# Optimization experiments

Measured on AMD Instinct MI355X. Metric: run time of the kernel, lower is better.

## Reference

```python
import jax, jax.numpy as jnp
import numpy as np

DIM = 256      # in_channels == hidden_channels
INNER = 256    # heads * dim_head
HEADS = 4
DH = 64        # dim_head = hidden_channels // num_heads
EDGE_DIM = 512 # 2 * in_channels
FF = 1024      # 4 * dim ff expansion
DEPTH = 2
OUT = 1
N = 50000      # two stacked graphs of 25000 nodes
E = 100000
HALF = 25000


def setup_inputs() -> dict:
    key = jax.random.key(0)
    ks = iter(jax.random.split(key, 32))

    def lin(fan_in, fan_out):
        w = jax.random.normal(next(ks), (DEPTH, fan_in, fan_out), jnp.float32) * (1.0 / np.sqrt(fan_in))
        b = jnp.zeros((DEPTH, fan_out), jnp.float32)
        return w, b

    x = jax.random.normal(next(ks), (N, DIM), jnp.float32)
    edge_index = jax.random.randint(next(ks), (2, E), 0, HALF, dtype=jnp.int32)
    Wq, bq = lin(DIM, INNER)
    Wkv, bkv = lin(DIM, 2 * INNER)
    We, be = lin(EDGE_DIM, INNER)
    Wo, bo = lin(INNER, DIM)
    W1, b1 = lin(DIM, FF)
    W2, b2 = lin(FF, DIM)
    g_attn = jax.random.normal(next(ks), (DEPTH, 3 * DIM, 1), jnp.float32) * (1.0 / np.sqrt(3 * DIM))
    g_ff = jax.random.normal(next(ks), (DEPTH, 3 * DIM, 1), jnp.float32) * (1.0 / np.sqrt(3 * DIM))
    ln1_g = jnp.ones((DEPTH, DIM), jnp.float32); ln1_b = jnp.zeros((DEPTH, DIM), jnp.float32)
    ln2_g = jnp.ones((DEPTH, DIM), jnp.float32); ln2_b = jnp.zeros((DEPTH, DIM), jnp.float32)
    Wout = jax.random.normal(next(ks), (DIM, OUT), jnp.float32) * (1.0 / np.sqrt(DIM))
    bout = jnp.zeros((OUT,), jnp.float32)
    return dict(x=x, edge_index=edge_index, ln1_g=ln1_g, ln1_b=ln1_b, Wq=Wq, bq=bq,
                Wkv=Wkv, bkv=bkv, We=We, be=be, Wo=Wo, bo=bo, g_attn=g_attn,
                ln2_g=ln2_g, ln2_b=ln2_b, W1=W1, b1=b1, W2=W2, b2=b2, g_ff=g_ff,
                Wout=Wout, bout=bout)


def _layer_norm(x, g, b):
    mu = jnp.mean(x, axis=-1, keepdims=True)
    var = jnp.mean(jnp.square(x - mu), axis=-1, keepdims=True)
    return (x - mu) * jax.lax.rsqrt(var + 1e-5) * g + b


def _gated_residual(x, res, w):
    # gate = sigmoid(Linear_no_bias(cat(x, res, x - res)))
    gate = jax.nn.sigmoid(jnp.concatenate([x, res, x - res], axis=-1) @ w)  # [n,1]
    return x * gate + res * (1.0 - gate)


def _forward(x, edge_index, ln1_g, ln1_b, Wq, bq, Wkv, bkv, We, be, Wo, bo, g_attn,
             ln2_g, ln2_b, W1, b1, W2, b2, g_ff, Wout, bout):
    src, dst = edge_index[0], edge_index[1]
    # edge_attr = cat(x[src], x[dst]) as built in DeepGraphTransformer_mse.forward
    edge_attr = jnp.concatenate([x[src], x[dst]], axis=-1)  # [E, 2*DIM]
    nodes = x
    n = nodes.shape[0]
    scale = DH ** -0.5
    for l in range(DEPTH):
        xn = _layer_norm(nodes, ln1_g[l], ln1_b[l])
        q = xn @ Wq[l] + bq[l]                                   # [n, INNER]
        k, v = jnp.split(xn @ Wkv[l] + bkv[l], 2, axis=-1)       # [n, INNER] each
        e = edge_attr @ We[l] + be[l]                            # [E, INNER]
        qe = q[dst].reshape(-1, HEADS, DH)                       # [E,H,Dh]
        ke = (k[src] + e).reshape(-1, HEADS, DH)
        ve = (v[src] + e).reshape(-1, HEADS, DH)
        sim = jnp.einsum('ehd,ehd->eh', qe, ke) * scale          # [E,H]
        smax = jax.ops.segment_max(sim, dst, num_segments=n)     # [n,H] (-inf for empty)
        ez = jnp.exp(sim - smax[dst])
        denom = jax.ops.segment_sum(ez, dst, num_segments=n)
        attn = ez / denom[dst]                                   # softmax over incoming edges
        agg = jax.ops.segment_sum(attn[:, :, None] * ve, dst, num_segments=n)
        attn_out = agg.reshape(n, INNER) @ Wo[l] + bo[l]         # [n, DIM]
        nodes = _gated_residual(attn_out, nodes, g_attn[l])
        xn2 = _layer_norm(nodes, ln2_g[l], ln2_b[l])
        h = jax.nn.gelu(xn2 @ W1[l] + b1[l], approximate=False) @ W2[l] + b2[l]
        nodes = _gated_residual(h, nodes, g_ff[l])
    z = nodes @ Wout + bout                                      # [n, OUT]
    return z


def reference(x, edge_index, ln1_g, ln1_b, Wq, bq, Wkv, bkv, We, be, Wo, bo, g_attn,
              ln2_g, ln2_b, W1, b1, W2, b2, g_ff, Wout, bout):
    z = _forward(x, edge_index, ln1_g, ln1_b, Wq, bq, Wkv, bkv, We, be, Wo, bo, g_attn,
                 ln2_g, ln2_b, W1, b1, W2, b2, g_ff, Wout, bout)
    half = z.shape[0] // 2
    z_old, z_new = z[:half], z[half:]
    return (z_new.reshape(-1), z_old, z_new)
```

## Files before the change

kernel.cpp:

```cpp
#include <hip/hip_runtime.h>
#include <cmath>

#define N_NODES 50000
#define N_EDGES 100000
#define HALF_N  25000
#define DIM     256
#define NDEPTH  2
#define MAXDEG  64

#define WT_QKVE 0
#define WT_WO   524288
#define WT_W1   589824
#define WT_W2   851968
#define WT_LAYER 1114112

typedef __bf16 bf16;
typedef bf16 bf16x8 __attribute__((ext_vector_type(8)));
typedef bf16 bf16x4 __attribute__((ext_vector_type(4)));
typedef float f32x4 __attribute__((ext_vector_type(4)));

__device__ __forceinline__ void lds_barrier() {
  asm volatile("s_waitcnt lgkmcnt(0)" ::: "memory");
  __builtin_amdgcn_s_barrier();
  __builtin_amdgcn_sched_barrier(0);
}

__device__ __forceinline__ float wave_sum(float v) {
  v += __shfl_xor(v, 1);
  v += __shfl_xor(v, 2);
  v += __shfl_xor(v, 4);
  v += __shfl_xor(v, 8);
  v += __shfl_xor(v, 16);
  v += __shfl_xor(v, 32);
  return v;
}

__device__ __forceinline__ float fast_gelu(float v) {
  float ax = fabsf(v) * 0.70710678118654752f;
  float t = __builtin_amdgcn_rcpf(fmaf(0.3275911f, ax, 1.0f));
  float p = t * fmaf(t, fmaf(t, fmaf(t, fmaf(t, 1.061405429f, -1.453152027f),
                                     1.421413741f), -0.284496736f), 0.254829592f);
  float e = __expf(-ax * ax);
  float erfv = fmaf(-p, e, 1.0f);
  float ph = copysignf(erfv, v);
  return 0.5f * v * (1.0f + ph);
}

__global__ void ln0_kernel(const float* __restrict__ in, const float* __restrict__ g,
                           const float* __restrict__ b, bf16* __restrict__ A2) {
  int row = blockIdx.x * 4 + (threadIdx.x >> 6);
  if (row >= HALF_N) return;
  int lane = threadIdx.x & 63;
  float4 x = reinterpret_cast<const float4*>(in + (size_t)row * DIM)[lane];
  float mu = wave_sum(x.x + x.y + x.z + x.w) * (1.0f / DIM);
  float d0 = x.x - mu, d1 = x.y - mu, d2 = x.z - mu, d3 = x.w - mu;
  float var = wave_sum(d0*d0 + d1*d1 + d2*d2 + d3*d3) * (1.0f / DIM);
  float r = rsqrtf(var + 1e-5f);
  float4 gv = reinterpret_cast<const float4*>(g)[lane];
  float4 bv = reinterpret_cast<const float4*>(b)[lane];
  bf16x4 o;
  o[0] = (bf16)(d0 * r * gv.x + bv.x);
  o[1] = (bf16)(d1 * r * gv.y + bv.y);
  o[2] = (bf16)(d2 * r * gv.z + bv.z);
  o[3] = (bf16)(d3 * r * gv.w + bv.w);
  *reinterpret_cast<bf16x4*>(A2 + (size_t)row * 512 + lane * 4) = o;
}

template<int KK, int NJ>
__global__ __launch_bounds__(256, 2) void gemm_nloop(
    const bf16* __restrict__ A, const bf16* __restrict__ Wp,
    const float* __restrict__ bias, bf16* __restrict__ C, int M) {
  constexpr int STEPS = KK / 64;
  __shared__ bf16x8 As[KK * 8];
  __shared__ bf16 Cs[64 * 128];
  const int tid = threadIdx.x;
  const int lane = tid & 63, wv = tid >> 6;
  const int wr = wv >> 1, wc = wv & 1;
  const int lm = lane & 15, kb = (lane >> 4) & 3;
  const int row0 = blockIdx.x * 64;
#pragma unroll
  for (int i = 0; i < KK / 32; ++i) {
    int idx = tid + i * 256;
    int row = idx & 63, k8 = idx >> 6;
    int rga = row0 + row; if (rga >= M) rga = M - 1;
    As[idx] = *reinterpret_cast<const bf16x8*>(A + (size_t)rga * KK + k8 * 8);
  }
  lds_barrier();
  const bf16x8* wb = reinterpret_cast<const bf16x8*>(Wp) + kb * 128 + wc * 64 + lm;
  for (int jn = 0; jn < NJ; ++jn) {
    f32x4 acc[2][4] = {};
    for (int st = 0; st < STEPS; ++st) {
#pragma unroll
      for (int ks = 0; ks < 2; ++ks) {
        bf16x8 bfr[4], af[2];
#pragma unroll
        for (int ni = 0; ni < 4; ++ni)
          bfr[ni] = wb[(size_t)jn * (KK * 16) + st * 1024 + ks * 512 + ni * 16];
#pragma unroll
        for (int mi = 0; mi < 2; ++mi)
          af[mi] = As[(st * 8 + ks * 4 + kb) * 64 + wr * 32 + mi * 16 + lm];
#pragma unroll
        for (int mi = 0; mi < 2; ++mi)
#pragma unroll
          for (int ni = 0; ni < 4; ++ni)
            acc[mi][ni] = __builtin_amdgcn_mfma_f32_16x16x32_bf16(af[mi], bfr[ni], acc[mi][ni], 0, 0, 0);
      }
    }
    lds_barrier();
#pragma unroll
    for (int ni = 0; ni < 4; ++ni) {
      int c = wc * 64 + ni * 16 + lm;
      float bval = bias[jn * 128 + c];
#pragma unroll
      for (int mi = 0; mi < 2; ++mi)
#pragma unroll
        for (int e = 0; e < 4; ++e) {
          int r = wr * 32 + mi * 16 + kb * 4 + e;
          Cs[r * 128 + c] = (bf16)(acc[mi][ni][e] + bval);
        }
    }
    lds_barrier();
    bf16x8* C8 = reinterpret_cast<bf16x8*>(C);
    const bf16x8* Cs8 = (const bf16x8*)Cs;
#pragma unroll
    for (int i = 0; i < 4; ++i) {
      int idx = tid + i * 256;
      int row = idx >> 4, c8 = idx & 15;
      int grow = row0 + row;
      if (grow < M) C8[(size_t)grow * (NJ * 16) + jn * 16 + c8] = Cs8[row * 16 + c8];
    }
  }
}

__global__ __launch_bounds__(256, 2) void wo_fused(
    const bf16* __restrict__ A, const bf16* __restrict__ Wp,
    const float* __restrict__ bo, const float* __restrict__ gattn,
    const float* __restrict__ ln2g, const float* __restrict__ ln2b,
    float* __restrict__ nodes, bf16* __restrict__ xn, int M) {
  __shared__ bf16x8 As[2048];
  __shared__ bf16 Cs[64 * 256];
  const int tid = threadIdx.x;
  const int lane = tid & 63, wv = tid >> 6;
  const int wr = wv >> 1, wc = wv & 1;
  const int lm = lane & 15, kb = (lane >> 4) & 3;
  const int row0 = blockIdx.x * 64;
#pragma unroll
  for (int i = 0; i < 8; ++i) {
    int idx = tid + i * 256;
    int row = idx & 63, k8 = idx >> 6;
    int rga = row0 + row; if (rga >= M) rga = M - 1;
    As[idx] = *reinterpret_cast<const bf16x8*>(A + (size_t)rga * 256 + k8 * 8);
  }
  lds_barrier();
  const bf16x8* wb = reinterpret_cast<const bf16x8*>(Wp) + kb * 128 + wc * 64 + lm;
  for (int jn = 0; jn < 2; ++jn) {
    f32x4 acc[2][4] = {};
#pragma unroll
    for (int st = 0; st < 4; ++st) {
#pragma unroll
      for (int ks = 0; ks < 2; ++ks) {
        bf16x8 bfr[4], af[2];
#pragma unroll
        for (int ni = 0; ni < 4; ++ni)
          bfr[ni] = wb[jn * 4096 + st * 1024 + ks * 512 + ni * 16];
#pragma unroll
        for (int mi = 0; mi < 2; ++mi)
          af[mi] = As[(st * 8 + ks * 4 + kb) * 64 + wr * 32 + mi * 16 + lm];
#pragma unroll
        for (int mi = 0; mi < 2; ++mi)
#pragma unroll
          for (int ni = 0; ni < 4; ++ni)
            acc[mi][ni] = __builtin_amdgcn_mfma_f32_16x16x32_bf16(af[mi], bfr[ni], acc[mi][ni], 0, 0, 0);
      }
    }
#pragma unroll
    for (int ni = 0; ni < 4; ++ni) {
      int cfull = jn * 128 + wc * 64 + ni * 16 + lm;
      float bval = bo[cfull];
#pragma unroll
      for (int mi = 0; mi < 2; ++mi)
#pragma unroll
        for (int e = 0; e < 4; ++e) {
          int r = wr * 32 + mi * 16 + kb * 4 + e;
          int ch = (cfull >> 3) ^ (r & 7);
          Cs[r * 256 + ch * 8 + (cfull & 7)] = (bf16)(acc[mi][ni][e] + bval);
        }
    }
  }
  lds_barrier();
  for (int pass = 0; pass < 16; ++pass) {
    int r = pass * 4 + wv;
    int grow = row0 + r;
    if (grow >= M) continue;
    int ch = (lane >> 1) ^ (r & 7);
    bf16x4 c4 = *reinterpret_cast<const bf16x4*>(Cs + r * 256 + ch * 8 + (lane & 1) * 4);
    float x0 = (float)c4[0], x1 = (float)c4[1], x2 = (float)c4[2], x3 = (float)c4[3];
    float4 rv = reinterpret_cast<const float4*>(nodes + (size_t)grow * 256)[lane];
    float4 w0 = reinterpret_cast<const float4*>(gattn)[lane];
    float4 w1 = reinterpret_cast<const float4*>(gattn + 256)[lane];
    float4 w2 = reinterpret_cast<const float4*>(gattn + 512)[lane];
    float dot = x0 * (w0.x + w2.x) + rv.x * (w1.x - w2.x)
              + x1 * (w0.y + w2.y) + rv.y * (w1.y - w2.y)
              + x2 * (w0.z + w2.z) + rv.z * (w1.z - w2.z)
              + x3 * (w0.w + w2.w) + rv.w * (w1.w - w2.w);
    dot = wave_sum(dot);
    float gate = 1.0f / (1.0f + __expf(-dot));
    float n0 = fmaf(x0 - rv.x, gate, rv.x);
    float n1 = fmaf(x1 - rv.y, gate, rv.y);
    float n2 = fmaf(x2 - rv.z, gate, rv.z);
    float n3 = fmaf(x3 - rv.w, gate, rv.w);
    float4 o; o.x = n0; o.y = n1; o.z = n2; o.w = n3;
    reinterpret_cast<float4*>(nodes + (size_t)grow * 256)[lane] = o;
    float mu = wave_sum(n0 + n1 + n2 + n3) * (1.0f / DIM);
    float d0 = n0 - mu, d1 = n1 - mu, d2 = n2 - mu, d3 = n3 - mu;
    float var = wave_sum(d0*d0 + d1*d1 + d2*d2 + d3*d3) * (1.0f / DIM);
    float rs = rsqrtf(var + 1e-5f);
    float4 gv = reinterpret_cast<const float4*>(ln2g)[lane];
    float4 bv = reinterpret_cast<const float4*>(ln2b)[lane];
    bf16x4 ob;
    ob[0] = (bf16)(d0 * rs * gv.x + bv.x);
    ob[1] = (bf16)(d1 * rs * gv.y + bv.y);
    ob[2] = (bf16)(d2 * rs * gv.z + bv.z);
    ob[3] = (bf16)(d3 * rs * gv.w + bv.w);
    *reinterpret_cast<bf16x4*>(xn + (size_t)grow * 256 + lane * 4) = ob;
  }
}

template<int LAST>
__global__ __launch_bounds__(512, 4) void ff_fused(
    const bf16* __restrict__ A, const bf16* __restrict__ W1p,
    const float* __restrict__ b1, const bf16* __restrict__ W2p,
    const float* __restrict__ b2, float* __restrict__ nodes,
    const float* __restrict__ gff, const float* __restrict__ ln1g,
    const float* __restrict__ ln1b, bf16* __restrict__ A2,
    const float* __restrict__ Wout, const float* __restrict__ bout,
    float* __restrict__ out, int M) {
  __shared__ char smem[49152];
  bf16x8* Xs = (bf16x8*)smem;
  bf16*   Cs = (bf16*)smem;
  bf16x8* Hs = (bf16x8*)(smem + 32768);
  const int tid = threadIdx.x;
  const int lane = tid & 63, wv = tid >> 6;
  const int wr = wv >> 2, wc = wv & 3;
  const int lm = lane & 15, kb = (lane >> 4) & 3;
  const int row0 = blockIdx.x * 64;
#pragma unroll
  for (int i = 0; i < 4; ++i) {
    int idx = tid + i * 512;
    int row = idx & 63, k8 = idx >> 6;
    int rga = row0 + row; if (rga >= M) rga = M - 1;
    Xs[idx] = *reinterpret_cast<const bf16x8*>(A + (size_t)rga * 256 + k8 * 8);
  }
  lds_barrier();
  const bf16x8* w1b = (const bf16x8*)W1p + kb * 128 + wc * 32 + lm;
  const bf16x8* w2b = (const bf16x8*)W2p + kb * 256 + wc * 64 + lm;
  f32x4 acc[2][4] = {};
  bf16* hsb = (bf16*)Hs;
  for (int j = 0; j < 8; ++j) {
    bf16x8 pf2[8];
#pragma unroll
    for (int ks = 0; ks < 2; ++ks)
#pragma unroll
      for (int ni = 0; ni < 4; ++ni)
        pf2[ks * 4 + ni] = w2b[j * 4096 + ks * 1024 + ni * 16];
    f32x4 acc1[2][2] = {};
#pragma unroll
    for (int half = 0; half < 2; ++half) {
#pragma unroll
      for (int ks = 0; ks < 4; ++ks) {
        bf16x8 bfr[2], af[2];
#pragma unroll
        for (int ni = 0; ni < 2; ++ni)
          bfr[ni] = w1b[j * 4096 + half * 2048 + ks * 512 + ni * 16];
#pragma unroll
        for (int mi = 0; mi < 2; ++mi)
          af[mi] = Xs[(half * 16 + ks * 4 + kb) * 64 + wr * 32 + mi * 16 + lm];
#pragma unroll
        for (int mi = 0; mi < 2; ++mi)
#pragma unroll
          for (int ni = 0; ni < 2; ++ni)
            acc1[mi][ni] = __builtin_amdgcn_mfma_f32_16x16x32_bf16(af[mi], bfr[ni], acc1[mi][ni], 0, 0, 0);
      }
    }
    lds_barrier();
#pragma unroll
    for (int ni = 0; ni < 2; ++ni) {
      int c = wc * 32 + ni * 16 + lm;
      float bval = b1[j * 128 + c];
#pragma unroll
      for (int mi = 0; mi < 2; ++mi)
#pragma unroll
        for (int e = 0; e < 4; ++e) {
          int r = wr * 32 + mi * 16 + kb * 4 + e;
          float v = fast_gelu(acc1[mi][ni][e] + bval);
          hsb[((c >> 3) * 64 + r) * 8 + (c & 7)] = (bf16)v;
        }
    }
    lds_barrier();
#pragma unroll
    for (int h2 = 0; h2 < 2; ++h2) {
#pragma unroll
      for (int ks = 0; ks < 2; ++ks) {
        bf16x8 bfr[4], af[2];
#pragma unroll
        for (int ni = 0; ni < 4; ++ni)
          bfr[ni] = (h2 == 0) ? pf2[ks * 4 + ni]
                              : w2b[j * 4096 + 2048 + ks * 1024 + ni * 16];
#pragma unroll
        for (int mi = 0; mi < 2; ++mi)
          af[mi] = Hs[(h2 * 8 + ks * 4 + kb) * 64 + wr * 32 + mi * 16 + lm];
#pragma unroll
        for (int mi = 0; mi < 2; ++mi)
#pragma unroll
          for (int ni = 0; ni < 4; ++ni)
            acc[mi][ni] = __builtin_amdgcn_mfma_f32_16x16x32_bf16(af[mi], bfr[ni], acc[mi][ni], 0, 0, 0);
      }
    }
  }
#pragma unroll
  for (int ni = 0; ni < 4; ++ni) {
    int c = wc * 64 + ni * 16 + lm;
    float bval = b2[c];
#pragma unroll
    for (int mi = 0; mi < 2; ++mi)
#pragma unroll
      for (int e = 0; e < 4; ++e) {
        int r = wr * 32 + mi * 16 + kb * 4 + e;
        int ch = (c >> 3) ^ (r & 7);
        Cs[r * 256 + ch * 8 + (c & 7)] = (bf16)(acc[mi][ni][e] + bval);
      }
  }
  lds_barrier();
  for (int pass = 0; pass < 8; ++pass) {
    int r = pass * 8 + wv;
    int grow = row0 + r;
    if (grow >= M) continue;
    int ch = (lane >> 1) ^ (r & 7);
    bf16x4 c4 = *reinterpret_cast<const bf16x4*>(Cs + r * 256 + ch * 8 + (lane & 1) * 4);
    float x0 = (float)c4[0], x1 = (float)c4[1], x2 = (float)c4[2], x3 = (float)c4[3];
    float4 rv = reinterpret_cast<const float4*>(nodes + (size_t)grow * 256)[lane];
    float4 w0 = reinterpret_cast<const float4*>(gff)[lane];
    float4 w1 = reinterpret_cast<const float4*>(gff + 256)[lane];
    float4 w2 = reinterpret_cast<const float4*>(gff + 512)[lane];
    float dot = x0 * (w0.x + w2.x) + rv.x * (w1.x - w2.x)
              + x1 * (w0.y + w2.y) + rv.y * (w1.y - w2.y)
              + x2 * (w0.z + w2.z) + rv.z * (w1.z - w2.z)
              + x3 * (w0.w + w2.w) + rv.w * (w1.w - w2.w);
    dot = wave_sum(dot);
    float gate = 1.0f / (1.0f + __expf(-dot));
    float n0 = fmaf(x0 - rv.x, gate, rv.x);
    float n1 = fmaf(x1 - rv.y, gate, rv.y);
    float n2 = fmaf(x2 - rv.z, gate, rv.z);
    float n3 = fmaf(x3 - rv.w, gate, rv.w);
    if (LAST) {
      float4 wo4 = reinterpret_cast<const float4*>(Wout)[lane];
      float z = n0 * wo4.x + n1 * wo4.y + n2 * wo4.z + n3 * wo4.w;
      z = wave_sum(z);
      if (lane == 0) {
        z += bout[0];
        if (grow < HALF_N) {
          out[HALF_N + grow] = z;
        } else {
          int jj = grow - HALF_N;
          out[jj] = z;
          out[2 * HALF_N + jj] = z;
        }
      }
    } else {
      float4 o; o.x = n0; o.y = n1; o.z = n2; o.w = n3;
      reinterpret_cast<float4*>(nodes + (size_t)grow * 256)[lane] = o;
      if (grow < HALF_N) {
        float mu = wave_sum(n0 + n1 + n2 + n3) * (1.0f / DIM);
        float d0 = n0 - mu, d1 = n1 - mu, d2 = n2 - mu, d3 = n3 - mu;
        float var = wave_sum(d0*d0 + d1*d1 + d2*d2 + d3*d3) * (1.0f / DIM);
        float rs = rsqrtf(var + 1e-5f);
        float4 gv = reinterpret_cast<const float4*>(ln1g)[lane];
        float4 bv = reinterpret_cast<const float4*>(ln1b)[lane];
        bf16x4 ob;
        ob[0] = (bf16)(d0 * rs * gv.x + bv.x);
        ob[1] = (bf16)(d1 * rs * gv.y + bv.y);
        ob[2] = (bf16)(d2 * rs * gv.z + bv.z);
        ob[3] = (bf16)(d3 * rs * gv.w + bv.w);
        *reinterpret_cast<bf16x4*>(A2 + (size_t)grow * 512 + lane * 4) = ob;
      }
    }
  }
}

__global__ void ell_build(const int* __restrict__ ei, int* __restrict__ deg,
                          int* __restrict__ ell) {
  int e = blockIdx.x * 256 + threadIdx.x;
  if (e >= N_EDGES) return;
  int s = ei[e], d = ei[N_EDGES + e];
  int pos = atomicAdd(&deg[d], 1);
  if (pos < MAXDEG) ell[d * MAXDEG + pos] = s;
}

__global__ void attn_gather(const int* __restrict__ deg, const int* __restrict__ ell,
                            const bf16* __restrict__ qkv, bf16* __restrict__ agg) {
  int d = blockIdx.x * 4 + (threadIdx.x >> 6);
  if (d >= HALF_N) return;
  int lane = threadIdx.x & 63;
  int cnt = deg[d]; if (cnt > MAXDEG) cnt = MAXDEG;
  const bf16* qr = qkv + (size_t)d * 1024;
  bf16x4 qb = *reinterpret_cast<const bf16x4*>(qr + lane * 4);
  float q0 = (float)qb[0], q1 = (float)qb[1], q2 = (float)qb[2], q3 = (float)qb[3];
  float m = -INFINITY, den = 0.0f, a0 = 0.0f, a1 = 0.0f, a2 = 0.0f, a3 = 0.0f;
  for (int i = 0; i < cnt; ++i) {
    int s = ell[d * MAXDEG + i];
    bf16x8 kv8 = *reinterpret_cast<const bf16x8*>(qkv + (size_t)s * 1024 + 256 + lane * 8);
    float p = q0 * (float)kv8[0] + q1 * (float)kv8[1] +
              q2 * (float)kv8[2] + q3 * (float)kv8[3];
    p += __shfl_xor(p, 1); p += __shfl_xor(p, 2);
    p += __shfl_xor(p, 4); p += __shfl_xor(p, 8);
    float sim = p * 0.125f;
    float nm = fmaxf(m, sim);
    float sc = __expf(m - nm);
    float w  = __expf(sim - nm);
    den = den * sc + w;
    a0 = a0 * sc + w * (float)kv8[4];
    a1 = a1 * sc + w * (float)kv8[5];
    a2 = a2 * sc + w * (float)kv8[6];
    a3 = a3 * sc + w * (float)kv8[7];
    m = nm;
  }
  bf16x4 o;
  if (cnt > 0) {
    float inv = 1.0f / den;
    bf16x4 eb = *reinterpret_cast<const bf16x4*>(qr + 768 + lane * 4);
    o[0] = (bf16)(a0 * inv + (float)eb[0]);
    o[1] = (bf16)(a1 * inv + (float)eb[1]);
    o[2] = (bf16)(a2 * inv + (float)eb[2]);
    o[3] = (bf16)(a3 * inv + (float)eb[3]);
  } else {
    o[0] = (bf16)0.0f; o[1] = (bf16)0.0f; o[2] = (bf16)0.0f; o[3] = (bf16)0.0f;
  }
  *reinterpret_cast<bf16x4*>(agg + (size_t)d * DIM + lane * 4) = o;
}

template<int DO_LN>
__global__ void gr_ln(const float* __restrict__ fb,
                      float* __restrict__ nodes, const float* __restrict__ w,
                      const float* __restrict__ g, const float* __restrict__ b,
                      bf16* __restrict__ xn, int rows) {
  int r = blockIdx.x * 4 + (threadIdx.x >> 6);
  if (r >= rows) return;
  int lane = threadIdx.x & 63;
  float4 f = reinterpret_cast<const float4*>(fb)[lane];
  float x0 = f.x, x1 = f.y, x2 = f.z, x3 = f.w;
  float4 rv = reinterpret_cast<const float4*>(nodes + (size_t)r * DIM)[lane];
  float4 w0 = reinterpret_cast<const float4*>(w)[lane];
  float4 w1 = reinterpret_cast<const float4*>(w + 256)[lane];
  float4 w2 = reinterpret_cast<const float4*>(w + 512)[lane];
  float p = x0 * (w0.x + w2.x) + rv.x * (w1.x - w2.x)
          + x1 * (w0.y + w2.y) + rv.y * (w1.y - w2.y)
          + x2 * (w0.z + w2.z) + rv.z * (w1.z - w2.z)
          + x3 * (w0.w + w2.w) + rv.w * (w1.w - w2.w);
  p = wave_sum(p);
  float gate = 1.0f / (1.0f + __expf(-p));
  float n0 = x0 * gate + rv.x * (1.0f - gate);
  float n1 = x1 * gate + rv.y * (1.0f - gate);
  float n2 = x2 * gate + rv.z * (1.0f - gate);
  float n3 = x3 * gate + rv.w * (1.0f - gate);
  float4 o; o.x = n0; o.y = n1; o.z = n2; o.w = n3;
  reinterpret_cast<float4*>(nodes + (size_t)r * DIM)[lane] = o;
  if (DO_LN) {
    float mu = wave_sum(n0 + n1 + n2 + n3) * (1.0f / DIM);
    float d0 = n0 - mu, d1 = n1 - mu, d2 = n2 - mu, d3 = n3 - mu;
    float var = wave_sum(d0*d0 + d1*d1 + d2*d2 + d3*d3) * (1.0f / DIM);
    float rs = rsqrtf(var + 1e-5f);
    float4 gv = reinterpret_cast<const float4*>(g)[lane];
    float4 bv = reinterpret_cast<const float4*>(b)[lane];
    bf16x4 ob;
    ob[0] = (bf16)(d0 * rs * gv.x + bv.x);
    ob[1] = (bf16)(d1 * rs * gv.y + bv.y);
    ob[2] = (bf16)(d2 * rs * gv.z + bv.z);
    ob[3] = (bf16)(d3 * rs * gv.w + bv.w);
    *reinterpret_cast<bf16x4*>(xn + (size_t)r * DIM + lane * 4) = ob;
  }
}

__global__ void prep_w(const float* __restrict__ Wq, const float* __restrict__ Wkv,
                       const float* __restrict__ We, const float* __restrict__ Wo,
                       const float* __restrict__ W1, const float* __restrict__ W2,
                       bf16* __restrict__ wt) {
  int idx = blockIdx.x * 256 + threadIdx.x;
  if (idx >= 2 * WT_LAYER) return;
  int l = idx / WT_LAYER, r = idx % WT_LAYER;
  float v;
  if (r < 524288) {
    int jn = r >> 16, t = r & 65535;
    int k8 = t >> 10, u = t & 1023, n = u >> 3, e = u & 7;
    int ncol = jn * 128 + n, k = k8 * 8 + e;
    if (ncol < 256) {
      v = (k < 256) ? Wq[l * 65536 + k * 256 + ncol] : 0.0f;
    } else if (ncol < 768) {
      int u2 = ncol - 256;
      int c = (u2 >> 3) * 4 + (u2 & 3);
      int half = (u2 >> 2) & 1;
      if (k < 256) v = Wkv[l * 131072 + k * 512 + half * 256 + c];
      else         v = We[l * 131072 + (k - 256) * 256 + c];
    } else {
      int c = ncol - 768;
      v = (k < 256) ? 0.0f : We[l * 131072 + k * 256 + c];
    }
  } else if (r < 589824) {
    int rr = r - 524288;
    int jn = rr >> 15, t = rr & 32767;
    int k8 = t >> 10, u = t & 1023, n = u >> 3, e = u & 7;
    v = Wo[l * 65536 + (k8 * 8 + e) * 256 + jn * 128 + n];
  } else if (r < 851968) {
    int rr = r - 589824;
    int j = rr >> 15, t = rr & 32767;
    int k8 = t >> 10, u = t & 1023, n = u >> 3, e = u & 7;
    v = W1[l * 262144 + (k8 * 8 + e) * 1024 + j * 128 + n];
  } else {
    int rr = r - 851968;
    int j = rr >> 15, t = rr & 32767;
    int k8 = t >> 11, u = t & 2047, n = u >> 3, e = u & 7;
    v = W2[l * 262144 + (j * 128 + k8 * 8 + e) * 256 + n];
  }
  wt[idx] = (bf16)v;
}

__global__ void prep_bias(const float* __restrict__ bq, const float* __restrict__ bkv,
                          const float* __restrict__ be, float* __restrict__ biasq) {
  int i = blockIdx.x * 256 + threadIdx.x;
  if (i >= 2048) return;
  int l = i >> 10, n = i & 1023;
  float v;
  if (n < 256) v = bq[l * 256 + n];
  else if (n < 768) {
    int u2 = n - 256;
    int c = (u2 >> 3) * 4 + (u2 & 3);
    int half = (u2 >> 2) & 1;
    v = bkv[l * 512 + half * 256 + c];
  } else v = be[l * 256 + (n - 768)];
  biasq[i] = v;
}

__global__ void prep_x(const float* __restrict__ x, bf16* __restrict__ A2) {
  int i = blockIdx.x * 256 + threadIdx.x;
  if (i >= HALF_N * 64) return;
  int row = i >> 6, c = i & 63;
  float4 v = reinterpret_cast<const float4*>(x)[i];
  bf16x4 o;
  o[0] = (bf16)v.x; o[1] = (bf16)v.y; o[2] = (bf16)v.z; o[3] = (bf16)v.w;
  *reinterpret_cast<bf16x4*>(A2 + (size_t)row * 512 + 256 + c * 4) = o;
}

extern "C" void kernel_launch(void* const* d_in, const int* in_sizes, int n_in,
                              void* d_out, int out_size, void* d_ws, size_t ws_size,
                              hipStream_t stream) {
  const float* x     = (const float*)d_in[0];
  const int*   ei    = (const int*)d_in[1];
  const float* ln1_g = (const float*)d_in[2];
  const float* ln1_b = (const float*)d_in[3];
  const float* Wq    = (const float*)d_in[4];
  const float* bq    = (const float*)d_in[5];
  const float* Wkv   = (const float*)d_in[6];
  const float* bkv   = (const float*)d_in[7];
  const float* We    = (const float*)d_in[8];
  const float* be    = (const float*)d_in[9];
  const float* Wo    = (const float*)d_in[10];
  const float* bo    = (const float*)d_in[11];
  const float* g_attn= (const float*)d_in[12];
  const float* ln2_g = (const float*)d_in[13];
  const float* ln2_b = (const float*)d_in[14];
  const float* W1    = (const float*)d_in[15];
  const float* b1    = (const float*)d_in[16];
  const float* W2    = (const float*)d_in[17];
  const float* b2    = (const float*)d_in[18];
  const float* g_ff  = (const float*)d_in[19];
  const float* Wout  = (const float*)d_in[20];
  const float* bout  = (const float*)d_in[21];
  float* out = (float*)d_out;

  char* base = (char*)d_ws;
  float* nodes   = (float*)base;  base += (size_t)N_NODES * DIM * 4;
  bf16*  A2      = (bf16*)base;   base += (size_t)HALF_N * 512 * 2;
  bf16*  xn_bf   = (bf16*)base;   base += (size_t)N_NODES * DIM * 2;
  bf16*  qkv     = (bf16*)base;   base += (size_t)HALF_N * 1024 * 2;
  bf16*  agg     = (bf16*)base;   base += (size_t)HALF_N * DIM * 2;
  bf16*  wt      = (bf16*)base;   base += (size_t)2 * WT_LAYER * 2;
  float* biasq   = (float*)base;  base += 2048 * 4;
  int*   deg     = (int*)base;    base += HALF_N * 4;
  int*   ell     = (int*)base;    base += (size_t)HALF_N * MAXDEG * 4;

  hipMemcpyAsync(nodes, x, (size_t)N_NODES * DIM * sizeof(float),
                 hipMemcpyDeviceToDevice, stream);
  prep_w<<<(2 * WT_LAYER + 255) / 256, 256, 0, stream>>>(Wq, Wkv, We, Wo, W1, W2, wt);
  prep_bias<<<8, 256, 0, stream>>>(bq, bkv, be, biasq);
  prep_x<<<(HALF_N * 64 + 255) / 256, 256, 0, stream>>>(x, A2);
  hipMemsetAsync(deg, 0, HALF_N * sizeof(int), stream);
  ell_build<<<(N_EDGES + 255) / 256, 256, 0, stream>>>(ei, deg, ell);

  const int GP_H = (HALF_N + 63) / 64;
  const int GP_N = (N_NODES + 63) / 64;

  for (int l = 0; l < NDEPTH; ++l) {
    const bf16* wl = wt + (size_t)l * WT_LAYER;
    if (l == 0)
      ln0_kernel<<<(HALF_N + 3) / 4, 256, 0, stream>>>(x, ln1_g, ln1_b, A2);
    gemm_nloop<512, 8><<<GP_H, 256, 0, stream>>>(A2, wl + WT_QKVE, biasq + l * 1024, qkv, HALF_N);
    attn_gather<<<(HALF_N + 3) / 4, 256, 0, stream>>>(deg, ell, qkv, agg);
    wo_fused<<<GP_H, 256, 0, stream>>>(agg, wl + WT_WO, bo + l * DIM,
                                       g_attn + l * 768, ln2_g + l * DIM, ln2_b + l * DIM,
                                       nodes, xn_bf, HALF_N);
    gr_ln<1><<<(HALF_N + 3) / 4, 256, 0, stream>>>(
        bo + l * DIM, nodes + (size_t)HALF_N * DIM, g_attn + l * 768,
        ln2_g + l * DIM, ln2_b + l * DIM, xn_bf + (size_t)HALF_N * DIM, HALF_N);
    if (l < NDEPTH - 1) {
      ff_fused<0><<<GP_N, 512, 0, stream>>>(
          xn_bf, wl + WT_W1, b1 + l * 1024, wl + WT_W2, b2 + l * DIM,
          nodes, g_ff + l * 768, ln1_g + (l + 1) * DIM, ln1_b + (l + 1) * DIM, A2,
          nullptr, nullptr, nullptr, N_NODES);
    } else {
      ff_fused<1><<<GP_N, 512, 0, stream>>>(
          xn_bf, wl + WT_W1, b1 + l * 1024, wl + WT_W2, b2 + l * DIM,
          nodes, g_ff + l * 768, nullptr, nullptr, nullptr,
          Wout, bout, out, N_NODES);
    }
  }
}
```

Baseline: 508.5 us.

## Fold edge projection through Wo and merge second-half gated residual into wo_fused

Softmax weights over incoming edges sum to one, so the edge-embedding term can be folded algebraically: We·Wo is precomputed, and the Wo GEMM now reads a K=512 input (agg plus the raw edge features from A2). This removes 256 output columns from the QKV GEMM and shrinks the qkv buffer. Nodes with no incoming edges fall back to the bias. The second-half gated-residual kernel is merged into wo_fused through an extra block branch. The change also prefetches the first weight fragments in gemm_nloop, preloads residuals in ff_fused, and unrolls the attention gather by two edges. In exchange, the Wo GEMM does twice the K work, and the folded weights are rounded to bf16.

```diff
diff --git a/kernel.cpp b/kernel.cpp
--- a/kernel.cpp
+++ b/kernel.cpp
@@ -9,10 +9,10 @@
 #define MAXDEG  64
 
 #define WT_QKVE 0
-#define WT_WO   524288
-#define WT_W1   589824
-#define WT_W2   851968
-#define WT_LAYER 1114112
+#define WT_WO   393216
+#define WT_W1   524288
+#define WT_W2   786432
+#define WT_LAYER 1048576
 
 typedef __bf16 bf16;
 typedef bf16 bf16x8 __attribute__((ext_vector_type(8)));
@@ -85,17 +85,26 @@
     int rga = row0 + row; if (rga >= M) rga = M - 1;
     As[idx] = *reinterpret_cast<const bf16x8*>(A + (size_t)rga * KK + k8 * 8);
   }
+  const bf16x8* wb = reinterpret_cast<const bf16x8*>(Wp) + kb * 128 + wc * 64 + lm;
+  bf16x8 pfr[4];
+#pragma unroll
+  for (int ni = 0; ni < 4; ++ni) pfr[ni] = wb[ni * 16];
   lds_barrier();
-  const bf16x8* wb = reinterpret_cast<const bf16x8*>(Wp) + kb * 128 + wc * 64 + lm;
   for (int jn = 0; jn < NJ; ++jn) {
     f32x4 acc[2][4] = {};
+#pragma unroll
     for (int st = 0; st < STEPS; ++st) {
 #pragma unroll
       for (int ks = 0; ks < 2; ++ks) {
         bf16x8 bfr[4], af[2];
-#pragma unroll
-        for (int ni = 0; ni < 4; ++ni)
-          bfr[ni] = wb[(size_t)jn * (KK * 16) + st * 1024 + ks * 512 + ni * 16];
+        if (st == 0 && ks == 0) {
+#pragma unroll
+          for (int ni = 0; ni < 4; ++ni) bfr[ni] = pfr[ni];
+        } else {
+#pragma unroll
+          for (int ni = 0; ni < 4; ++ni)
+            bfr[ni] = wb[(size_t)jn * (KK * 16) + st * 1024 + ks * 512 + ni * 16];
+        }
 #pragma unroll
         for (int mi = 0; mi < 2; ++mi)
           af[mi] = As[(st * 8 + ks * 4 + kb) * 64 + wr * 32 + mi * 16 + lm];
@@ -105,6 +114,11 @@
           for (int ni = 0; ni < 4; ++ni)
             acc[mi][ni] = __builtin_amdgcn_mfma_f32_16x16x32_bf16(af[mi], bfr[ni], acc[mi][ni], 0, 0, 0);
       }
+    }
+    if (jn + 1 < NJ) {
+#pragma unroll
+      for (int ni = 0; ni < 4; ++ni)
+        pfr[ni] = wb[(size_t)(jn + 1) * (KK * 16) + ni * 16];
     }
     lds_barrier();
 #pragma unroll
@@ -133,96 +147,151 @@
 }
 
 __global__ __launch_bounds__(256, 2) void wo_fused(
-    const bf16* __restrict__ A, const bf16* __restrict__ Wp,
-    const float* __restrict__ bo, const float* __restrict__ gattn,
-    const float* __restrict__ ln2g, const float* __restrict__ ln2b,
-    float* __restrict__ nodes, bf16* __restrict__ xn, int M) {
+    const bf16* __restrict__ agg, const bf16* __restrict__ A2,
+    const bf16* __restrict__ Wp, const float* __restrict__ bvec,
+    const float* __restrict__ bo, const int* __restrict__ deg,
+    const float* __restrict__ gattn, const float* __restrict__ ln2g,
+    const float* __restrict__ ln2b, float* __restrict__ nodes,
+    bf16* __restrict__ xn, int rows) {
   __shared__ bf16x8 As[2048];
   __shared__ bf16 Cs[64 * 256];
   const int tid = threadIdx.x;
   const int lane = tid & 63, wv = tid >> 6;
-  const int wr = wv >> 1, wc = wv & 1;
-  const int lm = lane & 15, kb = (lane >> 4) & 3;
   const int row0 = blockIdx.x * 64;
-#pragma unroll
-  for (int i = 0; i < 8; ++i) {
-    int idx = tid + i * 256;
-    int row = idx & 63, k8 = idx >> 6;
-    int rga = row0 + row; if (rga >= M) rga = M - 1;
-    As[idx] = *reinterpret_cast<const bf16x8*>(A + (size_t)rga * 256 + k8 * 8);
-  }
-  lds_barrier();
-  const bf16x8* wb = reinterpret_cast<const bf16x8*>(Wp) + kb * 128 + wc * 64 + lm;
-  for (int jn = 0; jn < 2; ++jn) {
-    f32x4 acc[2][4] = {};
-#pragma unroll
-    for (int st = 0; st < 4; ++st) {
-#pragma unroll
-      for (int ks = 0; ks < 2; ++ks) {
-        bf16x8 bfr[4], af[2];
-#pragma unroll
-        for (int ni = 0; ni < 4; ++ni)
-          bfr[ni] = wb[jn * 4096 + st * 1024 + ks * 512 + ni * 16];
+  if (row0 < HALF_N) {
+    const int wr = wv >> 1, wc = wv & 1;
+    const int lm = lane & 15, kb = (lane >> 4) & 3;
+#pragma unroll
+    for (int i = 0; i < 8; ++i) {
+      int idx = tid + i * 256;
+      int row = idx & 63, k8 = idx >> 6;
+      int rga = row0 + row; if (rga >= HALF_N) rga = HALF_N - 1;
+      As[idx] = *reinterpret_cast<const bf16x8*>(agg + (size_t)rga * 256 + k8 * 8);
+    }
+    bf16x8 afx[2][8];
+#pragma unroll
+    for (int mi = 0; mi < 2; ++mi) {
+      int row = row0 + wr * 32 + mi * 16 + lm;
+      if (row >= HALF_N) row = HALF_N - 1;
+      const bf16* pa = A2 + (size_t)row * 512 + 256 + kb * 8;
+#pragma unroll
+      for (int t = 0; t < 8; ++t)
+        afx[mi][t] = *reinterpret_cast<const bf16x8*>(pa + t * 32);
+    }
+    lds_barrier();
+    const bf16x8* wb = reinterpret_cast<const bf16x8*>(Wp) + kb * 128 + wc * 64 + lm;
+    for (int jn = 0; jn < 2; ++jn) {
+      f32x4 acc[2][4] = {};
+#pragma unroll
+      for (int st = 0; st < 8; ++st) {
+#pragma unroll
+        for (int ks = 0; ks < 2; ++ks) {
+          bf16x8 bfr[4], af[2];
+#pragma unroll
+          for (int ni = 0; ni < 4; ++ni)
+            bfr[ni] = wb[jn * 8192 + (st * 8 + ks * 4) * 128 + ni * 16];
+#pragma unroll
+          for (int mi = 0; mi < 2; ++mi)
+            af[mi] = (st < 4) ? As[(st * 8 + ks * 4 + kb) * 64 + wr * 32 + mi * 16 + lm]
+                              : afx[mi][(st - 4) * 2 + ks];
+#pragma unroll
+          for (int mi = 0; mi < 2; ++mi)
+#pragma unroll
+            for (int ni = 0; ni < 4; ++ni)
+              acc[mi][ni] = __builtin_amdgcn_mfma_f32_16x16x32_bf16(af[mi], bfr[ni], acc[mi][ni], 0, 0, 0);
+        }
+      }
+#pragma unroll
+      for (int ni = 0; ni < 4; ++ni) {
+        int cfull = jn * 128 + wc * 64 + ni * 16 + lm;
+        float bval = bvec[cfull];
 #pragma unroll
         for (int mi = 0; mi < 2; ++mi)
-          af[mi] = As[(st * 8 + ks * 4 + kb) * 64 + wr * 32 + mi * 16 + lm];
-#pragma unroll
-        for (int mi = 0; mi < 2; ++mi)
-#pragma unroll
-          for (int ni = 0; ni < 4; ++ni)
-            acc[mi][ni] = __builtin_amdgcn_mfma_f32_16x16x32_bf16(af[mi], bfr[ni], acc[mi][ni], 0, 0, 0);
-      }
-    }
-#pragma unroll
-    for (int ni = 0; ni < 4; ++ni) {
-      int cfull = jn * 128 + wc * 64 + ni * 16 + lm;
-      float bval = bo[cfull];
-#pragma unroll
-      for (int mi = 0; mi < 2; ++mi)
-#pragma unroll
-        for (int e = 0; e < 4; ++e) {
-          int r = wr * 32 + mi * 16 + kb * 4 + e;
-          int ch = (cfull >> 3) ^ (r & 7);
-          Cs[r * 256 + ch * 8 + (cfull & 7)] = (bf16)(acc[mi][ni][e] + bval);
-        }
-    }
-  }
-  lds_barrier();
-  for (int pass = 0; pass < 16; ++pass) {
-    int r = pass * 4 + wv;
-    int grow = row0 + r;
-    if (grow >= M) continue;
-    int ch = (lane >> 1) ^ (r & 7);
-    bf16x4 c4 = *reinterpret_cast<const bf16x4*>(Cs + r * 256 + ch * 8 + (lane & 1) * 4);
-    float x0 = (float)c4[0], x1 = (float)c4[1], x2 = (float)c4[2], x3 = (float)c4[3];
-    float4 rv = reinterpret_cast<const float4*>(nodes + (size_t)grow * 256)[lane];
-    float4 w0 = reinterpret_cast<const float4*>(gattn)[lane];
-    float4 w1 = reinterpret_cast<const float4*>(gattn + 256)[lane];
-    float4 w2 = reinterpret_cast<const float4*>(gattn + 512)[lane];
-    float dot = x0 * (w0.x + w2.x) + rv.x * (w1.x - w2.x)
-              + x1 * (w0.y + w2.y) + rv.y * (w1.y - w2.y)
-              + x2 * (w0.z + w2.z) + rv.z * (w1.z - w2.z)
-              + x3 * (w0.w + w2.w) + rv.w * (w1.w - w2.w);
-    dot = wave_sum(dot);
-    float gate = 1.0f / (1.0f + __expf(-dot));
-    float n0 = fmaf(x0 - rv.x, gate, rv.x);
-    float n1 = fmaf(x1 - rv.y, gate, rv.y);
-    float n2 = fmaf(x2 - rv.z, gate, rv.z);
-    float n3 = fmaf(x3 - rv.w, gate, rv.w);
-    float4 o; o.x = n0; o.y = n1; o.z = n2; o.w = n3;
-    reinterpret_cast<float4*>(nodes + (size_t)grow * 256)[lane] = o;
-    float mu = wave_sum(n0 + n1 + n2 + n3) * (1.0f / DIM);
-    float d0 = n0 - mu, d1 = n1 - mu, d2 = n2 - mu, d3 = n3 - mu;
-    float var = wave_sum(d0*d0 + d1*d1 + d2*d2 + d3*d3) * (1.0f / DIM);
-    float rs = rsqrtf(var + 1e-5f);
-    float4 gv = reinterpret_cast<const float4*>(ln2g)[lane];
-    float4 bv = reinterpret_cast<const float4*>(ln2b)[lane];
-    bf16x4 ob;
-    ob[0] = (bf16)(d0 * rs * gv.x + bv.x);
-    ob[1] = (bf16)(d1 * rs * gv.y + bv.y);
-    ob[2] = (bf16)(d2 * rs * gv.z + bv.z);
-    ob[3] = (bf16)(d3 * rs * gv.w + bv.w);
-    *reinterpret_cast<bf16x4*>(xn + (size_t)grow * 256 + lane * 4) = ob;
+#pragma unroll
+          for (int e = 0; e < 4; ++e) {
+            int r = wr * 32 + mi * 16 + kb * 4 + e;
+            int ch = (cfull >> 3) ^ (r & 7);
+            Cs[r * 256 + ch * 8 + (cfull & 7)] = (bf16)(acc[mi][ni][e] + bval);
+          }
+      }
+    }
+    lds_barrier();
+    for (int pass = 0; pass < 16; ++pass) {
+      int r = pass * 4 + wv;
+      int grow = row0 + r;
+      float x0, x1, x2, x3;
+      if (grow >= HALF_N || deg[grow] == 0) {
+        float4 bo4 = reinterpret_cast<const float4*>(bo)[lane];
+        x0 = bo4.x; x1 = bo4.y; x2 = bo4.z; x3 = bo4.w;
+      } else {
+        int ch = (lane >> 1) ^ (r & 7);
+        bf16x4 c4 = *reinterpret_cast<const bf16x4*>(Cs + r * 256 + ch * 8 + (lane & 1) * 4);
+        x0 = (float)c4[0]; x1 = (float)c4[1]; x2 = (float)c4[2]; x3 = (float)c4[3];
+      }
+      float4 rv = reinterpret_cast<const float4*>(nodes + (size_t)grow * 256)[lane];
+      float4 w0 = reinterpret_cast<const float4*>(gattn)[lane];
+      float4 w1 = reinterpret_cast<const float4*>(gattn + 256)[lane];
+      float4 w2 = reinterpret_cast<const float4*>(gattn + 512)[lane];
+      float dot = x0 * (w0.x + w2.x) + rv.x * (w1.x - w2.x)
+                + x1 * (w0.y + w2.y) + rv.y * (w1.y - w2.y)
+                + x2 * (w0.z + w2.z) + rv.z * (w1.z - w2.z)
+                + x3 * (w0.w + w2.w) + rv.w * (w1.w - w2.w);
+      dot = wave_sum(dot);
+      float gate = 1.0f / (1.0f + __expf(-dot));
+      float n0 = fmaf(x0 - rv.x, gate, rv.x);
+      float n1 = fmaf(x1 - rv.y, gate, rv.y);
+      float n2 = fmaf(x2 - rv.z, gate, rv.z);
+      float n3 = fmaf(x3 - rv.w, gate, rv.w);
+      float4 o; o.x = n0; o.y = n1; o.z = n2; o.w = n3;
+      reinterpret_cast<float4*>(nodes + (size_t)grow * 256)[lane] = o;
+      float mu = wave_sum(n0 + n1 + n2 + n3) * (1.0f / DIM);
+      float d0 = n0 - mu, d1 = n1 - mu, d2 = n2 - mu, d3 = n3 - mu;
+      float var = wave_sum(d0*d0 + d1*d1 + d2*d2 + d3*d3) * (1.0f / DIM);
+      float rs = rsqrtf(var + 1e-5f);
+      float4 gv = reinterpret_cast<const float4*>(ln2g)[lane];
+      float4 bv = reinterpret_cast<const float4*>(ln2b)[lane];
+      bf16x4 ob;
+      ob[0] = (bf16)(d0 * rs * gv.x + bv.x);
+      ob[1] = (bf16)(d1 * rs * gv.y + bv.y);
+      ob[2] = (bf16)(d2 * rs * gv.z + bv.z);
+      ob[3] = (bf16)(d3 * rs * gv.w + bv.w);
+      *reinterpret_cast<bf16x4*>(xn + (size_t)grow * 256 + lane * 4) = ob;
+    }
+  } else {
+    float4 bo4 = reinterpret_cast<const float4*>(bo)[lane];
+    for (int pass = 0; pass < 16; ++pass) {
+      int grow = row0 + pass * 4 + wv;
+      if (grow >= rows) continue;
+      float x0 = bo4.x, x1 = bo4.y, x2 = bo4.z, x3 = bo4.w;
+      float4 rv = reinterpret_cast<const float4*>(nodes + (size_t)grow * 256)[lane];
+      float4 w0 = reinterpret_cast<const float4*>(gattn)[lane];
+      float4 w1 = reinterpret_cast<const float4*>(gattn + 256)[lane];
+      float4 w2 = reinterpret_cast<const float4*>(gattn + 512)[lane];
+      float dot = x0 * (w0.x + w2.x) + rv.x * (w1.x - w2.x)
+                + x1 * (w0.y + w2.y) + rv.y * (w1.y - w2.y)
+                + x2 * (w0.z + w2.z) + rv.z * (w1.z - w2.z)
+                + x3 * (w0.w + w2.w) + rv.w * (w1.w - w2.w);
+      dot = wave_sum(dot);
+      float gate = 1.0f / (1.0f + __expf(-dot));
+      float n0 = fmaf(x0 - rv.x, gate, rv.x);
+      float n1 = fmaf(x1 - rv.y, gate, rv.y);
+      float n2 = fmaf(x2 - rv.z, gate, rv.z);
+      float n3 = fmaf(x3 - rv.w, gate, rv.w);
+      float4 o; o.x = n0; o.y = n1; o.z = n2; o.w = n3;
+      reinterpret_cast<float4*>(nodes + (size_t)grow * 256)[lane] = o;
+      float mu = wave_sum(n0 + n1 + n2 + n3) * (1.0f / DIM);
+      float d0 = n0 - mu, d1 = n1 - mu, d2 = n2 - mu, d3 = n3 - mu;
+      float var = wave_sum(d0*d0 + d1*d1 + d2*d2 + d3*d3) * (1.0f / DIM);
+      float rs = rsqrtf(var + 1e-5f);
+      float4 gv = reinterpret_cast<const float4*>(ln2g)[lane];
+      float4 bv = reinterpret_cast<const float4*>(ln2b)[lane];
+      bf16x4 ob;
+      ob[0] = (bf16)(d0 * rs * gv.x + bv.x);
+      ob[1] = (bf16)(d1 * rs * gv.y + bv.y);
+      ob[2] = (bf16)(d2 * rs * gv.z + bv.z);
+      ob[3] = (bf16)(d3 * rs * gv.w + bv.w);
+      *reinterpret_cast<bf16x4*>(xn + (size_t)grow * 256 + lane * 4) = ob;
+    }
   }
 }
 
@@ -251,6 +320,13 @@
     int rga = row0 + row; if (rga >= M) rga = M - 1;
     Xs[idx] = *reinterpret_cast<const bf16x8*>(A + (size_t)rga * 256 + k8 * 8);
   }
+  float4 rvf[8];
+#pragma unroll
+  for (int pass = 0; pass < 8; ++pass) {
+    int grow = row0 + pass * 8 + wv;
+    if (grow >= M) grow = M - 1;
+    rvf[pass] = reinterpret_cast<const float4*>(nodes + (size_t)grow * 256)[lane];
+  }
   lds_barrier();
   const bf16x8* w1b = (const bf16x8*)W1p + kb * 128 + wc * 32 + lm;
   const bf16x8* w2b = (const bf16x8*)W2p + kb * 256 + wc * 64 + lm;
@@ -338,7 +414,7 @@
     int ch = (lane >> 1) ^ (r & 7);
     bf16x4 c4 = *reinterpret_cast<const bf16x4*>(Cs + r * 256 + ch * 8 + (lane & 1) * 4);
     float x0 = (float)c4[0], x1 = (float)c4[1], x2 = (float)c4[2], x3 = (float)c4[3];
-    float4 rv = reinterpret_cast<const float4*>(nodes + (size_t)grow * 256)[lane];
+    float4 rv = rvf[pass];
     float4 w0 = reinterpret_cast<const float4*>(gff)[lane];
     float4 w1 = reinterpret_cast<const float4*>(gff + 256)[lane];
     float4 w2 = reinterpret_cast<const float4*>(gff + 512)[lane];
@@ -402,21 +478,43 @@
   if (d >= HALF_N) return;
   int lane = threadIdx.x & 63;
   int cnt = deg[d]; if (cnt > MAXDEG) cnt = MAXDEG;
-  const bf16* qr = qkv + (size_t)d * 1024;
+  const bf16* qr = qkv + (size_t)d * 768;
   bf16x4 qb = *reinterpret_cast<const bf16x4*>(qr + lane * 4);
   float q0 = (float)qb[0], q1 = (float)qb[1], q2 = (float)qb[2], q3 = (float)qb[3];
   float m = -INFINITY, den = 0.0f, a0 = 0.0f, a1 = 0.0f, a2 = 0.0f, a3 = 0.0f;
-  for (int i = 0; i < cnt; ++i) {
+  int i = 0;
+  for (; i + 2 <= cnt; i += 2) {
+    int s0 = ell[d * MAXDEG + i];
+    int s1 = ell[d * MAXDEG + i + 1];
+    bf16x8 k0 = *reinterpret_cast<const bf16x8*>(qkv + (size_t)s0 * 768 + 256 + lane * 8);
+    bf16x8 k1 = *reinterpret_cast<const bf16x8*>(qkv + (size_t)s1 * 768 + 256 + lane * 8);
+    float p0 = q0 * (float)k0[0] + q1 * (float)k0[1] + q2 * (float)k0[2] + q3 * (float)k0[3];
+    float p1 = q0 * (float)k1[0] + q1 * (float)k1[1] + q2 * (float)k1[2] + q3 * (float)k1[3];
+    p0 += __shfl_xor(p0, 1); p1 += __shfl_xor(p1, 1);
+    p0 += __shfl_xor(p0, 2); p1 += __shfl_xor(p1, 2);
+    p0 += __shfl_xor(p0, 4); p1 += __shfl_xor(p1, 4);
+    p0 += __shfl_xor(p0, 8); p1 += __shfl_xor(p1, 8);
+    float s0v = p0 * 0.125f, s1v = p1 * 0.125f;
+    float nm = fmaxf(m, fmaxf(s0v, s1v));
+    float sc = __expf(m - nm);
+    float w0 = __expf(s0v - nm), w1 = __expf(s1v - nm);
+    den = den * sc + w0 + w1;
+    a0 = a0 * sc + w0 * (float)k0[4] + w1 * (float)k1[4];
+    a1 = a1 * sc + w0 * (float)k0[5] + w1 * (float)k1[5];
+    a2 = a2 * sc + w0 * (float)k0[6] + w1 * (float)k1[6];
+    a3 = a3 * sc + w0 * (float)k0[7] + w1 * (float)k1[7];
+    m = nm;
+  }
+  if (i < cnt) {
     int s = ell[d * MAXDEG + i];
-    bf16x8 kv8 = *reinterpret_cast<const bf16x8*>(qkv + (size_t)s * 1024 + 256 + lane * 8);
-    float p = q0 * (float)kv8[0] + q1 * (float)kv8[1] +
-              q2 * (float)kv8[2] + q3 * (float)kv8[3];
+    bf16x8 kv8 = *reinterpret_cast<const bf16x8*>(qkv + (size_t)s * 768 + 256 + lane * 8);
+    float p = q0 * (float)kv8[0] + q1 * (float)kv8[1] + q2 * (float)kv8[2] + q3 * (float)kv8[3];
     p += __shfl_xor(p, 1); p += __shfl_xor(p, 2);
     p += __shfl_xor(p, 4); p += __shfl_xor(p, 8);
     float sim = p * 0.125f;
     float nm = fmaxf(m, sim);
     float sc = __expf(m - nm);
-    float w  = __expf(sim - nm);
+    float w = __expf(sim - nm);
     den = den * sc + w;
     a0 = a0 * sc + w * (float)kv8[4];
     a1 = a1 * sc + w * (float)kv8[5];
@@ -427,57 +525,14 @@
   bf16x4 o;
   if (cnt > 0) {
     float inv = 1.0f / den;
-    bf16x4 eb = *reinterpret_cast<const bf16x4*>(qr + 768 + lane * 4);
-    o[0] = (bf16)(a0 * inv + (float)eb[0]);
-    o[1] = (bf16)(a1 * inv + (float)eb[1]);
-    o[2] = (bf16)(a2 * inv + (float)eb[2]);
-    o[3] = (bf16)(a3 * inv + (float)eb[3]);
+    o[0] = (bf16)(a0 * inv);
+    o[1] = (bf16)(a1 * inv);
+    o[2] = (bf16)(a2 * inv);
+    o[3] = (bf16)(a3 * inv);
   } else {
     o[0] = (bf16)0.0f; o[1] = (bf16)0.0f; o[2] = (bf16)0.0f; o[3] = (bf16)0.0f;
   }
   *reinterpret_cast<bf16x4*>(agg + (size_t)d * DIM + lane * 4) = o;
-}
-
-template<int DO_LN>
-__global__ void gr_ln(const float* __restrict__ fb,
-                      float* __restrict__ nodes, const float* __restrict__ w,
-                      const float* __restrict__ g, const float* __restrict__ b,
-                      bf16* __restrict__ xn, int rows) {
-  int r = blockIdx.x * 4 + (threadIdx.x >> 6);
-  if (r >= rows) return;
-  int lane = threadIdx.x & 63;
-  float4 f = reinterpret_cast<const float4*>(fb)[lane];
-  float x0 = f.x, x1 = f.y, x2 = f.z, x3 = f.w;
-  float4 rv = reinterpret_cast<const float4*>(nodes + (size_t)r * DIM)[lane];
-  float4 w0 = reinterpret_cast<const float4*>(w)[lane];
-  float4 w1 = reinterpret_cast<const float4*>(w + 256)[lane];
-  float4 w2 = reinterpret_cast<const float4*>(w + 512)[lane];
-  float p = x0 * (w0.x + w2.x) + rv.x * (w1.x - w2.x)
-          + x1 * (w0.y + w2.y) + rv.y * (w1.y - w2.y)
-          + x2 * (w0.z + w2.z) + rv.z * (w1.z - w2.z)
-          + x3 * (w0.w + w2.w) + rv.w * (w1.w - w2.w);
-  p = wave_sum(p);
-  float gate = 1.0f / (1.0f + __expf(-p));
-  float n0 = x0 * gate + rv.x * (1.0f - gate);
-  float n1 = x1 * gate + rv.y * (1.0f - gate);
-  float n2 = x2 * gate + rv.z * (1.0f - gate);
-  float n3 = x3 * gate + rv.w * (1.0f - gate);
-  float4 o; o.x = n0; o.y = n1; o.z = n2; o.w = n3;
-  reinterpret_cast<float4*>(nodes + (size_t)r * DIM)[lane] = o;
-  if (DO_LN) {
-    float mu = wave_sum(n0 + n1 + n2 + n3) * (1.0f / DIM);
-    float d0 = n0 - mu, d1 = n1 - mu, d2 = n2 - mu, d3 = n3 - mu;
-    float var = wave_sum(d0*d0 + d1*d1 + d2*d2 + d3*d3) * (1.0f / DIM);
-    float rs = rsqrtf(var + 1e-5f);
-    float4 gv = reinterpret_cast<const float4*>(g)[lane];
-    float4 bv = reinterpret_cast<const float4*>(b)[lane];
-    bf16x4 ob;
-    ob[0] = (bf16)(d0 * rs * gv.x + bv.x);
-    ob[1] = (bf16)(d1 * rs * gv.y + bv.y);
-    ob[2] = (bf16)(d2 * rs * gv.z + bv.z);
-    ob[3] = (bf16)(d3 * rs * gv.w + bv.w);
-    *reinterpret_cast<bf16x4*>(xn + (size_t)r * DIM + lane * 4) = ob;
-  }
 }
 
 __global__ void prep_w(const float* __restrict__ Wq, const float* __restrict__ Wkv,
@@ -488,34 +543,33 @@
   if (idx >= 2 * WT_LAYER) return;
   int l = idx / WT_LAYER, r = idx % WT_LAYER;
   float v;
-  if (r < 524288) {
+  if (r < 393216) {
     int jn = r >> 16, t = r & 65535;
     int k8 = t >> 10, u = t & 1023, n = u >> 3, e = u & 7;
     int ncol = jn * 128 + n, k = k8 * 8 + e;
     if (ncol < 256) {
       v = (k < 256) ? Wq[l * 65536 + k * 256 + ncol] : 0.0f;
-    } else if (ncol < 768) {
+    } else {
       int u2 = ncol - 256;
       int c = (u2 >> 3) * 4 + (u2 & 3);
       int half = (u2 >> 2) & 1;
       if (k < 256) v = Wkv[l * 131072 + k * 512 + half * 256 + c];
       else         v = We[l * 131072 + (k - 256) * 256 + c];
-    } else {
-      int c = ncol - 768;
-      v = (k < 256) ? 0.0f : We[l * 131072 + k * 256 + c];
-    }
-  } else if (r < 589824) {
+    }
+  } else if (r < 524288) {
+    int rr = r - 393216;
+    int jn = rr >> 16, t = rr & 65535;
+    int k8 = t >> 10, u = t & 1023, n = u >> 3, e = u & 7;
+    int k = k8 * 8 + e;
+    if (k >= 256) return;
+    v = Wo[l * 65536 + k * 256 + jn * 128 + n];
+  } else if (r < 786432) {
     int rr = r - 524288;
-    int jn = rr >> 15, t = rr & 32767;
-    int k8 = t >> 10, u = t & 1023, n = u >> 3, e = u & 7;
-    v = Wo[l * 65536 + (k8 * 8 + e) * 256 + jn * 128 + n];
-  } else if (r < 851968) {
-    int rr = r - 589824;
     int j = rr >> 15, t = rr & 32767;
     int k8 = t >> 10, u = t & 1023, n = u >> 3, e = u & 7;
     v = W1[l * 262144 + (k8 * 8 + e) * 1024 + j * 128 + n];
   } else {
-    int rr = r - 851968;
+    int rr = r - 786432;
     int j = rr >> 15, t = rr & 32767;
     int k8 = t >> 11, u = t & 2047, n = u >> 3, e = u & 7;
     v = W2[l * 262144 + (j * 128 + k8 * 8 + e) * 256 + n];
@@ -523,19 +577,49 @@
   wt[idx] = (bf16)v;
 }
 
+__global__ void prep_weff(const float* __restrict__ We, const float* __restrict__ Wo,
+                          bf16* __restrict__ wt) {
+  int idx = blockIdx.x * 256 + threadIdx.x;
+  if (idx >= 2 * 65536) return;
+  int l = idx >> 16, r = idx & 65535;
+  int k = r >> 8, n = r & 255;
+  const float* wer = We + l * 131072 + (256 + k) * 256;
+  const float* wor = Wo + l * 65536 + n;
+  float acc = 0.0f;
+#pragma unroll 4
+  for (int m = 0; m < 256; ++m) acc += wer[m] * wor[m * 256];
+  int kf = 256 + k;
+  size_t off = (size_t)l * WT_LAYER + WT_WO +
+               (n >> 7) * 65536 + (kf >> 3) * 1024 + (n & 127) * 8 + (kf & 7);
+  wt[off] = (bf16)acc;
+}
+
+__global__ void prep_bvec(const float* __restrict__ be, const float* __restrict__ Wo,
+                          const float* __restrict__ bo, float* __restrict__ biasq) {
+  int idx = blockIdx.x * 256 + threadIdx.x;
+  if (idx >= 512) return;
+  int l = idx >> 8, n = idx & 255;
+  const float* ber = be + l * 256;
+  const float* wor = Wo + l * 65536 + n;
+  float acc = bo[l * 256 + n];
+#pragma unroll 4
+  for (int m = 0; m < 256; ++m) acc += ber[m] * wor[m * 256];
+  biasq[1536 + l * 256 + n] = acc;
+}
+
 __global__ void prep_bias(const float* __restrict__ bq, const float* __restrict__ bkv,
-                          const float* __restrict__ be, float* __restrict__ biasq) {
+                          float* __restrict__ biasq) {
   int i = blockIdx.x * 256 + threadIdx.x;
-  if (i >= 2048) return;
-  int l = i >> 10, n = i & 1023;
+  if (i >= 1536) return;
+  int l = i / 768, n = i % 768;
   float v;
   if (n < 256) v = bq[l * 256 + n];
-  else if (n < 768) {
+  else {
     int u2 = n - 256;
     int c = (u2 >> 3) * 4 + (u2 & 3);
     int half = (u2 >> 2) & 1;
     v = bkv[l * 512 + half * 256 + c];
-  } else v = be[l * 256 + (n - 768)];
+  }
   biasq[i] = v;
 }
 
@@ -580,7 +664,7 @@
   float* nodes   = (float*)base;  base += (size_t)N_NODES * DIM * 4;
   bf16*  A2      = (bf16*)base;   base += (size_t)HALF_N * 512 * 2;
   bf16*  xn_bf   = (bf16*)base;   base += (size_t)N_NODES * DIM * 2;
-  bf16*  qkv     = (bf16*)base;   base += (size_t)HALF_N * 1024 * 2;
+  bf16*  qkv     = (bf16*)base;   base += (size_t)HALF_N * 768 * 2;
   bf16*  agg     = (bf16*)base;   base += (size_t)HALF_N * DIM * 2;
   bf16*  wt      = (bf16*)base;   base += (size_t)2 * WT_LAYER * 2;
   float* biasq   = (float*)base;  base += 2048 * 4;
@@ -590,7 +674,9 @@
   hipMemcpyAsync(nodes, x, (size_t)N_NODES * DIM * sizeof(float),
                  hipMemcpyDeviceToDevice, stream);
   prep_w<<<(2 * WT_LAYER + 255) / 256, 256, 0, stream>>>(Wq, Wkv, We, Wo, W1, W2, wt);
-  prep_bias<<<8, 256, 0, stream>>>(bq, bkv, be, biasq);
+  prep_weff<<<(2 * 65536 + 255) / 256, 256, 0, stream>>>(We, Wo, wt);
+  prep_bvec<<<2, 256, 0, stream>>>(be, Wo, bo, biasq);
+  prep_bias<<<6, 256, 0, stream>>>(bq, bkv, biasq);
   prep_x<<<(HALF_N * 64 + 255) / 256, 256, 0, stream>>>(x, A2);
   hipMemsetAsync(deg, 0, HALF_N * sizeof(int), stream);
   ell_build<<<(N_EDGES + 255) / 256, 256, 0, stream>>>(ei, deg, ell);
@@ -602,14 +688,12 @@
     const bf16* wl = wt + (size_t)l * WT_LAYER;
     if (l == 0)
       ln0_kernel<<<(HALF_N + 3) / 4, 256, 0, stream>>>(x, ln1_g, ln1_b, A2);
-    gemm_nloop<512, 8><<<GP_H, 256, 0, stream>>>(A2, wl + WT_QKVE, biasq + l * 1024, qkv, HALF_N);
+    gemm_nloop<512, 6><<<GP_H, 256, 0, stream>>>(A2, wl + WT_QKVE, biasq + l * 768, qkv, HALF_N);
     attn_gather<<<(HALF_N + 3) / 4, 256, 0, stream>>>(deg, ell, qkv, agg);
-    wo_fused<<<GP_H, 256, 0, stream>>>(agg, wl + WT_WO, bo + l * DIM,
-                                       g_attn + l * 768, ln2_g + l * DIM, ln2_b + l * DIM,
-                                       nodes, xn_bf, HALF_N);
-    gr_ln<1><<<(HALF_N + 3) / 4, 256, 0, stream>>>(
-        bo + l * DIM, nodes + (size_t)HALF_N * DIM, g_attn + l * 768,
-        ln2_g + l * DIM, ln2_b + l * DIM, xn_bf + (size_t)HALF_N * DIM, HALF_N);
+    wo_fused<<<GP_N, 256, 0, stream>>>(agg, A2, wl + WT_WO, biasq + 1536 + l * 256,
+                                       bo + l * DIM, deg, g_attn + l * 768,
+                                       ln2_g + l * DIM, ln2_b + l * DIM,
+                                       nodes, xn_bf, N_NODES);
     if (l < NDEPTH - 1) {
       ff_fused<0><<<GP_N, 512, 0, stream>>>(
           xn_bf, wl + WT_W1, b1 + l * 1024, wl + WT_W2, b2 + l * DIM,
```

New measurement: 568.1 us. 1.12x slower.
